# Performance work log

Hardware: AMD Instinct MI355X
Metric: run time of the kernel (lower is better)

The kernel has to match this reference:

```python
import jax, jax.numpy as jnp
import numpy as np

H = 50  # hidden_size

def setup_inputs() -> dict:
    key = jax.random.key(0)
    ks = jax.random.split(key, 7)
    B, T, I = 8192, 2048, 1
    s_ih = 1.0 / np.sqrt(H)
    x = jax.random.normal(ks[0], (B, T, I), dtype=jnp.float32)
    # PyTorch nn.LSTM params, gate order (i, f, g, o)
    W_ih = jax.random.uniform(ks[1], (4 * H, I), minval=-s_ih, maxval=s_ih, dtype=jnp.float32)
    W_hh = jax.random.uniform(ks[2], (4 * H, H), minval=-s_ih, maxval=s_ih, dtype=jnp.float32)
    b_ih = jax.random.uniform(ks[3], (4 * H,), minval=-s_ih, maxval=s_ih, dtype=jnp.float32)
    b_hh = jax.random.uniform(ks[4], (4 * H,), minval=-s_ih, maxval=s_ih, dtype=jnp.float32)
    W_lin = jax.random.uniform(ks[5], (1, H), minval=-s_ih, maxval=s_ih, dtype=jnp.float32)
    b_lin = jax.random.uniform(ks[6], (1,), minval=-s_ih, maxval=s_ih, dtype=jnp.float32)
    return {"x": x, "W_ih": W_ih, "W_hh": W_hh, "b_ih": b_ih, "b_hh": b_hh,
            "W_lin": W_lin, "b_lin": b_lin}

def _lstm_last_h(x, W_ih, W_hh, b_ih, b_hh):
    B = x.shape[0]
    # precompute input contribution per timestep: [T, B, 4H]
    xg = jnp.einsum('bti,gi->tbg', x, W_ih) + (b_ih + b_hh)  # [T,B,4H]

    def step(carry, xg_t):
        h, c = carry
        z = xg_t + h @ W_hh.T  # [B,4H]
        i = jax.nn.sigmoid(z[:, :H])
        f = jax.nn.sigmoid(z[:, H:2 * H])
        g = jnp.tanh(z[:, 2 * H:3 * H])
        o = jax.nn.sigmoid(z[:, 3 * H:])
        c = f * c + i * g
        h = o * jnp.tanh(c)
        return (h, c), None

    h0 = jnp.zeros((B, H), dtype=x.dtype)
    c0 = jnp.zeros((B, H), dtype=x.dtype)
    (h_last, _), _ = jax.lax.scan(step, (h0, c0), xg)
    return h_last  # [B,H]

def reference(x, W_ih, W_hh, b_ih, b_hh, W_lin, b_lin):
    h_last = _lstm_last_h(x, W_ih, W_hh, b_ih, b_hh)
    return h_last @ W_lin.T + b_lin  # [B,1]
```

## Files before the change

kernel.cpp:

```cpp
#include <hip/hip_runtime.h>


#define HID   50
#define NSTEP 2048
#define BPB   16
#define HSTR  72

typedef _Float16 half8   __attribute__((ext_vector_type(8)));
typedef float    float4v __attribute__((ext_vector_type(4)));
typedef float    float2v __attribute__((ext_vector_type(2)));

__device__ __forceinline__ float2v lo2(float4v v) { float2v r; r[0] = v[0]; r[1] = v[1]; return r; }
__device__ __forceinline__ float2v hi2(float4v v) { float2v r; r[0] = v[2]; r[1] = v[3]; return r; }

__device__ __forceinline__ float2v exp2v(float2v x) {
    float2v r;
    r[0] = __builtin_amdgcn_exp2f(x[0]);
    r[1] = __builtin_amdgcn_exp2f(x[1]);
    return r;
}

__device__ __forceinline__ float2v gate_pairs2(float2v zi, float2v zf, float2v zg,
                                               float2v zo, float2v& c) {
    float2v ei = exp2v(zi);
    float2v ef = exp2v(zf);
    float2v Eg = exp2v(zg);
    float2v eo = exp2v(zo);
    float2v t1  = (1.0f + ei) * (1.0f + Eg);
    float2v pf  = 1.0f + ef;
    float2v num = c * t1 + pf * (Eg - 1.0f);
    float2v D   = t1 * pf;
    float   rP  = __builtin_amdgcn_rcpf(D[0] * D[1]);
    float2v Dsw; Dsw[0] = D[1]; Dsw[1] = D[0];
    c = num * Dsw * rP;
    float2v a = 2.8853900817779268f * c;
    a[0] = fminf(fmaxf(a[0], -24.0f), 24.0f);
    a[1] = fminf(fmaxf(a[1], -24.0f), 24.0f);
    float2v Ec  = exp2v(a);
    float2v den = (1.0f + eo) * (1.0f + Ec);
    float   rQ  = __builtin_amdgcn_rcpf(den[0] * den[1]);
    float2v dsw; dsw[0] = den[1]; dsw[1] = den[0];
    return (Ec - 1.0f) * dsw * rQ;
}

__global__ __launch_bounds__(256, 2) void lstm_fused(
    const float* __restrict__ x,
    const float* __restrict__ W_ih,
    const float* __restrict__ W_hh,
    const float* __restrict__ b_ih,
    const float* __restrict__ b_hh,
    const float* __restrict__ W_lin,
    const float* __restrict__ b_lin,
    float* __restrict__ out)
{
    __shared__ __align__(16) _Float16 hbuf[2][BPB][HSTR];

    const int tid  = threadIdx.x;
    const int wave = tid >> 6;
    const int lane = tid & 63;
    const int col  = lane & 15;
    const int quad = lane >> 4;
    const int b0   = blockIdx.x * BPB;
    const int j    = wave * 16 + col;

    for (int i = tid; i < 2 * BPB * HSTR; i += 256)
        (&hbuf[0][0][0])[i] = (_Float16)0.0f;
    __syncthreads();
    if (tid < BPB) {
        hbuf[0][tid][HID]     = (_Float16)x[(size_t)(b0 + tid) * NSTEP];
        hbuf[0][tid][HID + 1] = (_Float16)1.0f;
        hbuf[1][tid][HID + 1] = (_Float16)1.0f;
    }

    const float LOG2E = 1.4426950408889634f;
    half8 bfrag[4][2];
    for (int g = 0; g < 4; ++g) {
        const float sc = (g == 2) ? (2.0f * LOG2E) : (-LOG2E);
        for (int kt = 0; kt < 2; ++kt) {
            half8 f;
            #pragma unroll
            for (int jj = 0; jj < 8; ++jj) {
                int k = kt * 32 + quad * 8 + jj;
                float v = 0.0f;
                if (j < HID) {
                    int row = g * HID + j;
                    if (k < HID)           v = W_hh[row * HID + k];
                    else if (k == HID)     v = W_ih[row];
                    else if (k == HID + 1) v = b_ih[row] + b_hh[row];
                }
                f[jj] = (_Float16)(v * sc);
            }
            bfrag[g][kt] = f;
        }
    }

    float2v c01 = {0.f, 0.f};
    float2v c23 = {0.f, 0.f};
    const bool xloader = (wave == 3) && (quad == 0);
    const float* xrow = x + (size_t)(b0 + col) * NSTEP;
    const float4v Z4 = {0.f, 0.f, 0.f, 0.f};

    float xn_reg = 0.f;
    if (xloader)
        xn_reg = xrow[1 < NSTEP ? 1 : NSTEP - 1];

    __syncthreads();

    if (blockIdx.x & 1) {
        __builtin_amdgcn_s_sleep(15);
    }

#define STEP(CUR, NXT, T)                                                        \
    {                                                                            \
                    \
        if (xloader)                                                             \
            hbuf[NXT][col][HID] = (_Float16)xn_reg;                              \
        float xn_new = 0.f;                                                      \
        if (xloader) {                                                           \
            int tt = (T) + 2;                                                    \
            if (tt > NSTEP - 1) tt = NSTEP - 1;                                  \
            xn_new = xrow[tt];                                                   \
        }                                                                        \
        const _Float16* arow = &hbuf[CUR][col][0];                               \
        half8 a0 = *(const half8*)(arow + quad * 8);                             \
        half8 a1 = *(const half8*)(arow + 32 + quad * 8);                        \
        float4v d0, d1, d2, d3;                                                  \
        d0 = __builtin_amdgcn_mfma_f32_16x16x32_f16(a0, bfrag[0][0], Z4, 0, 0, 0); \
        d1 = __builtin_amdgcn_mfma_f32_16x16x32_f16(a0, bfrag[1][0], Z4, 0, 0, 0); \
        d2 = __builtin_amdgcn_mfma_f32_16x16x32_f16(a0, bfrag[2][0], Z4, 0, 0, 0); \
        d3 = __builtin_amdgcn_mfma_f32_16x16x32_f16(a0, bfrag[3][0], Z4, 0, 0, 0); \
        d0 = __builtin_amdgcn_mfma_f32_16x16x32_f16(a1, bfrag[0][1], d0, 0, 0, 0); \
        d1 = __builtin_amdgcn_mfma_f32_16x16x32_f16(a1, bfrag[1][1], d1, 0, 0, 0); \
        d2 = __builtin_amdgcn_mfma_f32_16x16x32_f16(a1, bfrag[2][1], d2, 0, 0, 0); \
        d3 = __builtin_amdgcn_mfma_f32_16x16x32_f16(a1, bfrag[3][1], d3, 0, 0, 0); \
                        \
        __builtin_amdgcn_s_setprio(1);                                           \
                   \
        float2v h01 = gate_pairs2(lo2(d0), lo2(d1), lo2(d2), lo2(d3), c01);      \
        if (j < HID) {                                                           \
            hbuf[NXT][quad * 4 + 0][j] = (_Float16)h01[0];                       \
            hbuf[NXT][quad * 4 + 1][j] = (_Float16)h01[1];                       \
        }                                                                        \
        float2v h23 = gate_pairs2(hi2(d0), hi2(d1), hi2(d2), hi2(d3), c23);      \
        if (j < HID) {                                                           \
            hbuf[NXT][quad * 4 + 2][j] = (_Float16)h23[0];                       \
            hbuf[NXT][quad * 4 + 3][j] = (_Float16)h23[1];                       \
        }                                                                        \
        __builtin_amdgcn_s_setprio(0);                                           \
        xn_reg = xn_new;                                                         \
        __syncthreads();                                                         \
    }

    for (int t = 0; t < NSTEP; t += 2) {
        STEP(0, 1, t)
        STEP(1, 0, t + 1)
    }
#undef STEP

    if (tid < BPB) {
        float s = b_lin[0];
        for (int k = 0; k < HID; ++k)
            s += (float)hbuf[0][tid][k] * W_lin[k];
        out[b0 + tid] = s;
    }
}

extern "C" void kernel_launch(void* const* d_in, const int* in_sizes, int n_in,
                              void* d_out, int out_size, void* d_ws, size_t ws_size,
                              hipStream_t stream) {
    const float* x     = (const float*)d_in[0];
    const float* W_ih  = (const float*)d_in[1];
    const float* W_hh  = (const float*)d_in[2];
    const float* b_ih  = (const float*)d_in[3];
    const float* b_hh  = (const float*)d_in[4];
    const float* W_lin = (const float*)d_in[5];
    const float* b_lin = (const float*)d_in[6];
    float* outp = (float*)d_out;
    dim3 grid(8192 / BPB), block(256);
    hipLaunchKernelGGL(lstm_fused, grid, block, 0, stream,
                       x, W_ih, W_hh, b_ih, b_hh, W_lin, b_lin, outp);
}
```

Before: 1.255 ms.

## Ping-pong two batch groups per block to overlap MFMA and gate phases

Each block now handles 32 batch rows as two 16-row groups of four waves each. In every half-step one group runs its MFMA phase while the other runs its gate transcendentals, then they swap, so matrix and vector work from different groups overlap within a CU. The h buffer is no longer double-buffered per group, because the barrier between phases provides the ordering. The cost is 512-thread blocks at one block per CU, two barriers per timestep instead of one, and removal of the staggered sleep.

Result: slower. 1.581 ms (+26.0%).

```diff
diff --git a/kernel.cpp b/kernel.cpp
--- a/kernel.cpp
+++ b/kernel.cpp
@@ -3,7 +3,7 @@
 
 #define HID   50
 #define NSTEP 2048
-#define BPB   16
+#define BPB   32
 #define HSTR  72
 
 typedef _Float16 half8   __attribute__((ext_vector_type(8)));
@@ -43,7 +43,7 @@
     return (Ec - 1.0f) * dsw * rQ;
 }
 
-__global__ __launch_bounds__(256, 2) void lstm_fused(
+__global__ __launch_bounds__(512, 1) void lstm_fused(
     const float* __restrict__ x,
     const float* __restrict__ W_ih,
     const float* __restrict__ W_hh,
@@ -53,23 +53,26 @@
     const float* __restrict__ b_lin,
     float* __restrict__ out)
 {
-    __shared__ __align__(16) _Float16 hbuf[2][BPB][HSTR];
+    __shared__ __align__(16) _Float16 hbuf[2][16][HSTR];
 
     const int tid  = threadIdx.x;
     const int wave = tid >> 6;
+    const int grp  = wave >> 2;
+    const int wv   = wave & 3;
     const int lane = tid & 63;
     const int col  = lane & 15;
     const int quad = lane >> 4;
-    const int b0   = blockIdx.x * BPB;
-    const int j    = wave * 16 + col;
+    const int bb   = blockIdx.x * BPB;
+    const int b0g  = bb + grp * 16;
+    const int j    = wv * 16 + col;
 
-    for (int i = tid; i < 2 * BPB * HSTR; i += 256)
+    for (int i = tid; i < 2 * 16 * HSTR; i += 512)
         (&hbuf[0][0][0])[i] = (_Float16)0.0f;
     __syncthreads();
     if (tid < BPB) {
-        hbuf[0][tid][HID]     = (_Float16)x[(size_t)(b0 + tid) * NSTEP];
-        hbuf[0][tid][HID + 1] = (_Float16)1.0f;
-        hbuf[1][tid][HID + 1] = (_Float16)1.0f;
+        int g = tid >> 4, r = tid & 15;
+        hbuf[g][r][HID]     = (_Float16)x[(size_t)(bb + tid) * NSTEP];
+        hbuf[g][r][HID + 1] = (_Float16)1.0f;
     }
 
     const float LOG2E = 1.4426950408889634f;
@@ -96,72 +99,85 @@
 
     float2v c01 = {0.f, 0.f};
     float2v c23 = {0.f, 0.f};
-    const bool xloader = (wave == 3) && (quad == 0);
-    const float* xrow = x + (size_t)(b0 + col) * NSTEP;
+    float4v z0, z1, z2, z3;
+    const bool xloader = (wv == 3) && (quad == 0);
+    const float* xrow = x + (size_t)(b0g + col) * NSTEP;
     const float4v Z4 = {0.f, 0.f, 0.f, 0.f};
 
     float xn_reg = 0.f;
     if (xloader)
-        xn_reg = xrow[1 < NSTEP ? 1 : NSTEP - 1];
+        xn_reg = xrow[1];
 
     __syncthreads();
 
-    if (blockIdx.x & 1) {
-        __builtin_amdgcn_s_sleep(15);
+#define MFMA_PHASE()                                                             \
+    {                                                                            \
+        const _Float16* arow = &hbuf[grp][col][0];                               \
+        half8 a0 = *(const half8*)(arow + quad * 8);                             \
+        half8 a1 = *(const half8*)(arow + 32 + quad * 8);                        \
+        z0 = __builtin_amdgcn_mfma_f32_16x16x32_f16(a0, bfrag[0][0], Z4, 0, 0, 0); \
+        z1 = __builtin_amdgcn_mfma_f32_16x16x32_f16(a0, bfrag[1][0], Z4, 0, 0, 0); \
+        z2 = __builtin_amdgcn_mfma_f32_16x16x32_f16(a0, bfrag[2][0], Z4, 0, 0, 0); \
+        z3 = __builtin_amdgcn_mfma_f32_16x16x32_f16(a0, bfrag[3][0], Z4, 0, 0, 0); \
+        z0 = __builtin_amdgcn_mfma_f32_16x16x32_f16(a1, bfrag[0][1], z0, 0, 0, 0); \
+        z1 = __builtin_amdgcn_mfma_f32_16x16x32_f16(a1, bfrag[1][1], z1, 0, 0, 0); \
+        z2 = __builtin_amdgcn_mfma_f32_16x16x32_f16(a1, bfrag[2][1], z2, 0, 0, 0); \
+        z3 = __builtin_amdgcn_mfma_f32_16x16x32_f16(a1, bfrag[3][1], z3, 0, 0, 0); \
     }
 
-#define STEP(CUR, NXT, T)                                                        \
+#define GATES_PHASE(T)                                                           \
     {                                                                            \
-                    \
         if (xloader)                                                             \
-            hbuf[NXT][col][HID] = (_Float16)xn_reg;                              \
+            hbuf[grp][col][HID] = (_Float16)xn_reg;                              \
         float xn_new = 0.f;                                                      \
         if (xloader) {                                                           \
             int tt = (T) + 2;                                                    \
             if (tt > NSTEP - 1) tt = NSTEP - 1;                                  \
             xn_new = xrow[tt];                                                   \
         }                                                                        \
-        const _Float16* arow = &hbuf[CUR][col][0];                               \
-        half8 a0 = *(const half8*)(arow + quad * 8);                             \
-        half8 a1 = *(const half8*)(arow + 32 + quad * 8);                        \
-        float4v d0, d1, d2, d3;                                                  \
-        d0 = __builtin_amdgcn_mfma_f32_16x16x32_f16(a0, bfrag[0][0], Z4, 0, 0, 0); \
-        d1 = __builtin_amdgcn_mfma_f32_16x16x32_f16(a0, bfrag[1][0], Z4, 0, 0, 0); \
-        d2 = __builtin_amdgcn_mfma_f32_16x16x32_f16(a0, bfrag[2][0], Z4, 0, 0, 0); \
-        d3 = __builtin_amdgcn_mfma_f32_16x16x32_f16(a0, bfrag[3][0], Z4, 0, 0, 0); \
-        d0 = __builtin_amdgcn_mfma_f32_16x16x32_f16(a1, bfrag[0][1], d0, 0, 0, 0); \
-        d1 = __builtin_amdgcn_mfma_f32_16x16x32_f16(a1, bfrag[1][1], d1, 0, 0, 0); \
-        d2 = __builtin_amdgcn_mfma_f32_16x16x32_f16(a1, bfrag[2][1], d2, 0, 0, 0); \
-        d3 = __builtin_amdgcn_mfma_f32_16x16x32_f16(a1, bfrag[3][1], d3, 0, 0, 0); \
-                        \
         __builtin_amdgcn_s_setprio(1);                                           \
-                   \
-        float2v h01 = gate_pairs2(lo2(d0), lo2(d1), lo2(d2), lo2(d3), c01);      \
+        float2v h01 = gate_pairs2(lo2(z0), lo2(z1), lo2(z2), lo2(z3), c01);      \
         if (j < HID) {                                                           \
-            hbuf[NXT][quad * 4 + 0][j] = (_Float16)h01[0];                       \
-            hbuf[NXT][quad * 4 + 1][j] = (_Float16)h01[1];                       \
+            hbuf[grp][quad * 4 + 0][j] = (_Float16)h01[0];                       \
+            hbuf[grp][quad * 4 + 1][j] = (_Float16)h01[1];                       \
         }                                                                        \
-        float2v h23 = gate_pairs2(hi2(d0), hi2(d1), hi2(d2), hi2(d3), c23);      \
+        float2v h23 = gate_pairs2(hi2(z0), hi2(z1), hi2(z2), hi2(z3), c23);      \
         if (j < HID) {                                                           \
-            hbuf[NXT][quad * 4 + 2][j] = (_Float16)h23[0];                       \
-            hbuf[NXT][quad * 4 + 3][j] = (_Float16)h23[1];                       \
+            hbuf[grp][quad * 4 + 2][j] = (_Float16)h23[0];                       \
+            hbuf[grp][quad * 4 + 3][j] = (_Float16)h23[1];                       \
         }                                                                        \
         __builtin_amdgcn_s_setprio(0);                                           \
         xn_reg = xn_new;                                                         \
-        __syncthreads();                                                         \
     }
 
-    for (int t = 0; t < NSTEP; t += 2) {
-        STEP(0, 1, t)
-        STEP(1, 0, t + 1)
+    if (grp == 1) {
+        MFMA_PHASE()
     }
-#undef STEP
+    __syncthreads();
+
+    for (int t = 0; t < NSTEP; ++t) {
+        if (grp == 0) {
+            MFMA_PHASE()
+        } else {
+            GATES_PHASE(t)
+        }
+        __syncthreads();
+        if (grp == 0) {
+            GATES_PHASE(t)
+        } else {
+            MFMA_PHASE()
+        }
+        __syncthreads();
+    }
+#undef MFMA_PHASE
+#undef GATES_PHASE
 
     if (tid < BPB) {
+        int g = tid >> 4, r = tid & 15;
         float s = b_lin[0];
         for (int k = 0; k < HID; ++k)
-            s += (float)hbuf[0][tid][k] * W_lin[k];
-        out[b0 + tid] = s;
+            s += (float)hbuf[g][r][k] * W_lin[k];
+        out[bb + tid] = s;
     }
 }
 
@@ -176,7 +192,7 @@
     const float* W_lin = (const float*)d_in[5];
     const float* b_lin = (const float*)d_in[6];
     float* outp = (float*)d_out;
-    dim3 grid(8192 / BPB), block(256);
+    dim3 grid(8192 / BPB), block(512);
     hipLaunchKernelGGL(lstm_fused, grid, block, 0, stream,
                        x, W_ih, W_hh, b_ih, b_hh, W_lin, b_lin, outp);
 }
```
